# Optimization experiments

Hardware: AMD Instinct MI355X
Metric: run time of the kernel (lower is better)

## Reference

```python
import jax, jax.numpy as jnp
import numpy as np

V, R, D, B, L, M = 10000, 8192, 1024, 1024, 64, 65536


def setup_inputs() -> dict:
    key = jax.random.key(0)
    ks = jax.random.split(key, 10)
    s = 1.0 / np.sqrt(D)
    tokens = jax.random.randint(ks[0], (B, L), 0, V)
    i_idx = jax.random.randint(ks[1], (M,), 0, B * L)
    j_idx = jax.random.randint(ks[2], (M,), 0, B * L)  # stands for j-1 in the original
    r_idx = jax.random.randint(ks[3], (M,), 0, R)
    emb = jax.random.normal(ks[4], (V, D), dtype=jnp.float32) * 0.1
    Wxh = jax.random.normal(ks[5], (D, D), dtype=jnp.float32) * s
    Whh = jax.random.normal(ks[6], (D, D), dtype=jnp.float32) * s
    bh = jnp.zeros((D,), jnp.float32)
    h0 = jnp.zeros((D,), jnp.float32)
    W1 = jax.random.normal(ks[7], (2 * D, D), dtype=jnp.float32) * (1.0 / np.sqrt(2 * D))
    b1 = jnp.zeros((D,), jnp.float32)
    W2 = jax.random.normal(ks[8], (D, R), dtype=jnp.float32) * s
    b2 = jnp.zeros((R,), jnp.float32)
    return dict(tokens=tokens, i_idx=i_idx, j_idx=j_idx, r_idx=r_idx, emb=emb,
                Wxh=Wxh, Whh=Whh, bh=bh, h0=h0, W1=W1, b1=b1, W2=W2, b2=b2)


def reference(tokens, i_idx, j_idx, r_idx, emb, Wxh, Whh, bh, h0, W1, b1, W2, b2):
    # encode: embedding lookup + Elman RNN over time (batched across B sentences)
    x = emb[tokens]                                   # [B, L, D]
    h_init = jnp.broadcast_to(h0, (x.shape[0], h0.shape[0]))

    def step(h, xt):                                  # xt: [B, D]
        h = jnp.tanh(xt @ Wxh + h @ Whh + bh)
        return h, h

    _, hs = jax.lax.scan(step, h_init, jnp.swapaxes(x, 0, 1))  # [L, B, D]
    enc = jnp.swapaxes(hs, 0, 1).reshape(-1, h0.shape[0])      # [B*L, D]

    # batched score_rule over all M tree nodes:
    # cat(enc[i], enc[j-1]) -> tanh(Linear) -> Linear, then index rule r
    c = jnp.concatenate([enc[i_idx], enc[j_idx]], axis=-1)     # [M, 2D]
    h = jnp.tanh(c @ W1 + b1)                                  # [M, D]
    w2_sel = W2.T[r_idx]                                       # [M, D] (only needed logit rows)
    scores = jnp.einsum('md,md->m', h, w2_sel) + b2[r_idx]     # [M]
    return scores
```

## Files before the change

### kernel.cpp

```cpp
#include <hip/hip_runtime.h>

#define D_DIM   1024
#define L_SEQ   64
#define B_BATCH 1024
#define M_NODES 65536
#define R_RULES 8192
#define V_VOCAB 10000

typedef unsigned short bf16_t;
typedef __attribute__((ext_vector_type(8))) short s8v;
typedef __attribute__((ext_vector_type(4))) short s4v;
typedef __attribute__((ext_vector_type(4))) float f4v;

static __device__ __forceinline__ float bf2f(unsigned short u) {
    union { unsigned int i; float f; } v; v.i = ((unsigned int)u) << 16; return v.f;
}
static __device__ __forceinline__ unsigned short f2bf(float f) {
    union { float f; unsigned int i; } v; v.f = f;
    return (unsigned short)((v.i + 0x7FFFu + ((v.i >> 16) & 1u)) >> 16);
}
static __device__ __forceinline__ float fast_tanh(float x) {
    float xc = fminf(fmaxf(x, -15.f), 15.f);
    float t  = __expf(2.f * xc);
    return (t - 1.f) * __builtin_amdgcn_rcpf(t + 1.f);
}

static __device__ __forceinline__ f4v mfma16(s8v a, s8v b, f4v c) {
    return __builtin_amdgcn_mfma_f32_16x16x32_bf16(a, b, c, 0, 0, 0);
}

__global__ __launch_bounds__(256) void k_cvt_emb(
    const float* __restrict__ emb, bf16_t* __restrict__ embB)
{
    size_t i = ((size_t)blockIdx.x * 256 + threadIdx.x) * 8;
    f4v x0 = *(const f4v*)&emb[i];
    f4v x1 = *(const f4v*)&emb[i + 4];
    s8v o;
    o[0] = (short)f2bf(x0.x); o[1] = (short)f2bf(x0.y);
    o[2] = (short)f2bf(x0.z); o[3] = (short)f2bf(x0.w);
    o[4] = (short)f2bf(x1.x); o[5] = (short)f2bf(x1.y);
    o[6] = (short)f2bf(x1.z); o[7] = (short)f2bf(x1.w);
    *(s8v*)&embB[i] = o;
}

__global__ __launch_bounds__(256) void k_transcvt(
    const float* __restrict__ src, bf16_t* __restrict__ dst, int K, int N)
{
    __shared__ float s[32][33];
    int n0 = blockIdx.x * 32, k0 = blockIdx.y * 32;
    int tx = threadIdx.x, ty = threadIdx.y;
#pragma unroll
    for (int i = 0; i < 4; ++i)
        s[ty + i * 8][tx] = src[(size_t)(k0 + ty + i * 8) * N + n0 + tx];
    __syncthreads();
#pragma unroll
    for (int i = 0; i < 4; ++i)
        dst[(size_t)(n0 + ty + i * 8) * K + k0 + tx] = f2bf(s[tx][ty + i * 8]);
}

__global__ __launch_bounds__(256) void k_cvt_h0(
    const float* __restrict__ h0, bf16_t* __restrict__ h0b)
{
    for (int u = threadIdx.x; u < D_DIM; u += 256) h0b[u] = f2bf(h0[u]);
}

__global__ __launch_bounds__(256) void k_xw_mfma(
    const int* __restrict__ tokens, const bf16_t* __restrict__ embB,
    const bf16_t* __restrict__ WxhT, const float* __restrict__ bh,
    bf16_t* __restrict__ XE)
{
    __shared__ bf16_t As[128 * 64];
    __shared__ bf16_t Bs[128 * 64];
    __shared__ float  epi[4][16][68];

    const int bi  = blockIdx.x;
    const int xcd = bi & 7, j = bi >> 3;
    const int row0 = ((xcd << 6) + (j >> 3)) * 128;
    const int col0 = (j & 7) * 128;

    const int tid = threadIdx.x;
    const int w = tid >> 6, l = tid & 63;
    const int q = l >> 4, t16 = l & 15;
    const int wm = (w >> 1) * 64, wn = (w & 1) * 64;

    const int rr = tid >> 2, c0 = tid & 3;
    const int sw0 = ((c0       ^ (rr & 7)) << 3);
    const int sw1 = (((c0 + 4) ^ (rr & 7)) << 3);

    const bf16_t* arow[2];
#pragma unroll
    for (int r = 0; r < 2; ++r)
        arow[r] = embB + (size_t)tokens[row0 + rr + r * 64] * D_DIM + c0 * 8;
    const bf16_t* brow[2];
#pragma unroll
    for (int r = 0; r < 2; ++r)
        brow[r] = WxhT + (size_t)(col0 + rr + r * 64) * D_DIM + c0 * 8;

    f4v acc[4][4];
#pragma unroll
    for (int i = 0; i < 4; ++i)
#pragma unroll
        for (int jj = 0; jj < 4; ++jj) acc[i][jj] = (f4v)0.f;

    s8v a00 = *(const s8v*)(arow[0]);
    s8v a01 = *(const s8v*)(arow[0] + 32);
    s8v a10 = *(const s8v*)(arow[1]);
    s8v a11 = *(const s8v*)(arow[1] + 32);
    s8v b00 = *(const s8v*)(brow[0]);
    s8v b01 = *(const s8v*)(brow[0] + 32);
    s8v b10 = *(const s8v*)(brow[1]);
    s8v b11 = *(const s8v*)(brow[1] + 32);

    const int r7 = t16 & 7;
    for (int k0 = 0; k0 < D_DIM; k0 += 64) {
        __syncthreads();
        *(s8v*)&As[rr * 64 + sw0]        = a00;
        *(s8v*)&As[rr * 64 + sw1]        = a01;
        *(s8v*)&As[(rr + 64) * 64 + sw0] = a10;
        *(s8v*)&As[(rr + 64) * 64 + sw1] = a11;
        *(s8v*)&Bs[rr * 64 + sw0]        = b00;
        *(s8v*)&Bs[rr * 64 + sw1]        = b01;
        *(s8v*)&Bs[(rr + 64) * 64 + sw0] = b10;
        *(s8v*)&Bs[(rr + 64) * 64 + sw1] = b11;
        int kn = k0 + 64;
        if (kn < D_DIM) {
            a00 = *(const s8v*)(arow[0] + kn);
            a01 = *(const s8v*)(arow[0] + kn + 32);
            a10 = *(const s8v*)(arow[1] + kn);
            a11 = *(const s8v*)(arow[1] + kn + 32);
            b00 = *(const s8v*)(brow[0] + kn);
            b01 = *(const s8v*)(brow[0] + kn + 32);
            b10 = *(const s8v*)(brow[1] + kn);
            b11 = *(const s8v*)(brow[1] + kn + 32);
        }
        __syncthreads();
#pragma unroll
        for (int sub = 0; sub < 2; ++sub) {
            const int rsl = (((sub * 4 + q) ^ r7) << 3);
            s8v af[4], bfr[4];
#pragma unroll
            for (int ti = 0; ti < 4; ++ti)
                af[ti] = *(const s8v*)&As[(wm + ti * 16 + t16) * 64 + rsl];
#pragma unroll
            for (int tj = 0; tj < 4; ++tj)
                bfr[tj] = *(const s8v*)&Bs[(wn + tj * 16 + t16) * 64 + rsl];
#pragma unroll
            for (int ti = 0; ti < 4; ++ti)
#pragma unroll
                for (int tj = 0; tj < 4; ++tj)
                    acc[ti][tj] = mfma16(af[ti], bfr[tj], acc[ti][tj]);
        }
    }

    const int lr = l >> 2, c16 = (l & 3) * 16;
    f4v bias[4];
#pragma unroll
    for (int u = 0; u < 4; ++u)
        bias[u] = *(const f4v*)&bh[col0 + wn + c16 + u * 4];
#pragma unroll
    for (int ti = 0; ti < 4; ++ti) {
#pragma unroll
        for (int tj = 0; tj < 4; ++tj)
#pragma unroll
            for (int rg = 0; rg < 4; ++rg)
                epi[w][q * 4 + rg][tj * 16 + t16] = acc[ti][tj][rg];
        s8v o0, o1;
#pragma unroll
        for (int u = 0; u < 8; ++u) {
            o0[u] = (short)f2bf(epi[w][lr][c16 + u]     + bias[u >> 2][u & 3]);
            o1[u] = (short)f2bf(epi[w][lr][c16 + 8 + u] + bias[2 + (u >> 2)][u & 3]);
        }
        size_t orow = (size_t)(row0 + wm + ti * 16 + lr) * D_DIM + col0 + wn + c16;
        *(s8v*)&XE[orow]     = o0;
        *(s8v*)&XE[orow + 8] = o1;
    }
}

__global__ __launch_bounds__(512) void k_step_mfma(
    const bf16_t* __restrict__ Abase, int strideRow,
    const bf16_t* __restrict__ WhhT, bf16_t* __restrict__ XE, int t)
{
    __shared__ bf16_t As[64 * 256];
    __shared__ bf16_t Bs[64 * 256];
    __shared__ float  epi[8][16][36];

    const int tid = threadIdx.x;
    const int w = tid >> 6, l = tid & 63;
    const int q = l >> 4, t16 = l & 15;
    const int wr = w & 3, wc = w >> 2;
    const int row0 = blockIdx.x * 64, col0 = blockIdx.y * 64;

    const int rr = tid >> 3, c0 = tid & 7;
    const int swb = ((c0 ^ (rr & 7)) << 3);

    const bf16_t* asrc = Abase + (size_t)(row0 + rr) * strideRow + c0 * 8;
    const bf16_t* bsrc = WhhT + (size_t)(col0 + rr) * D_DIM + c0 * 8;

    f4v acc[2];
    acc[0] = (f4v)0.f; acc[1] = (f4v)0.f;

    s8v pa[4], pb[4];
#pragma unroll
    for (int kk = 0; kk < 4; ++kk) {
        pa[kk] = *(const s8v*)(asrc + kk * 64);
        pb[kk] = *(const s8v*)(bsrc + kk * 64);
    }

    const int r7 = t16 & 7;
    for (int k0 = 0; k0 < D_DIM; k0 += 256) {
        __syncthreads();
#pragma unroll
        for (int kk = 0; kk < 4; ++kk) {
            *(s8v*)&As[rr * 256 + kk * 64 + swb] = pa[kk];
            *(s8v*)&Bs[rr * 256 + kk * 64 + swb] = pb[kk];
        }
        int kn = k0 + 256;
        if (kn < D_DIM) {
#pragma unroll
            for (int kk = 0; kk < 4; ++kk) {
                pa[kk] = *(const s8v*)(asrc + kn + kk * 64);
                pb[kk] = *(const s8v*)(bsrc + kn + kk * 64);
            }
        }
        __syncthreads();
#pragma unroll
        for (int sub = 0; sub < 8; ++sub) {
            const int slot = sub * 4 + q;
            const int rsl  = ((slot & 24) | ((slot ^ r7) & 7)) << 3;
            s8v af = *(const s8v*)&As[(wr * 16 + t16) * 256 + rsl];
            s8v b0 = *(const s8v*)&Bs[(wc * 32 + t16) * 256 + rsl];
            s8v b1 = *(const s8v*)&Bs[(wc * 32 + 16 + t16) * 256 + rsl];
            acc[0] = mfma16(af, b0, acc[0]);
            acc[1] = mfma16(af, b1, acc[1]);
        }
    }

    const int lr = l >> 2, c8 = (l & 3) * 8;
#pragma unroll
    for (int tj = 0; tj < 2; ++tj)
#pragma unroll
        for (int rg = 0; rg < 4; ++rg)
            epi[w][q * 4 + rg][tj * 16 + t16] = acc[tj][rg];
    f4v v0 = *(const f4v*)&epi[w][lr][c8];
    f4v v1 = *(const f4v*)&epi[w][lr][c8 + 4];
    int b = row0 + wr * 16 + lr;
    size_t xi = ((size_t)b * L_SEQ + t) * D_DIM + col0 + wc * 32 + c8;
    s8v x = *(const s8v*)&XE[xi];
    s8v o;
#pragma unroll
    for (int u = 0; u < 4; ++u) {
        o[u]     = (short)f2bf(fast_tanh(bf2f((unsigned short)x[u])     + v0[u]));
        o[u + 4] = (short)f2bf(fast_tanh(bf2f((unsigned short)x[u + 4]) + v1[u]));
    }
    *(s8v*)&XE[xi] = o;
}

__global__ __launch_bounds__(256) void k_mlp_mfma(
    const int* __restrict__ i_idx, const int* __restrict__ j_idx,
    const bf16_t* __restrict__ XE, const bf16_t* __restrict__ W1T,
    const float* __restrict__ b1, const bf16_t* __restrict__ Wt2,
    const int* __restrict__ r_idx, float* __restrict__ partials)
{
    __shared__ bf16_t As[128 * 64];
    __shared__ bf16_t Bs[128 * 64];

    const int bi  = blockIdx.x;
    const int xcd = bi & 7, j = bi >> 3;
    const int rowTile = (xcd << 6) + (j >> 3);
    const int colTile = j & 7;
    const int row0 = rowTile * 128, col0 = colTile * 128;

    const int tid = threadIdx.x;
    const int w = tid >> 6, l = tid & 63;
    const int q = l >> 4, t16 = l & 15;
    const int wm = (w >> 1) * 64, wn = (w & 1) * 64;

    const int rr = tid >> 2, c0 = tid & 3;
    const int sw0 = ((c0       ^ (rr & 7)) << 3);
    const int sw1 = (((c0 + 4) ^ (rr & 7)) << 3);

    const bf16_t* pi[2]; const bf16_t* pj[2];
#pragma unroll
    for (int r = 0; r < 2; ++r) {
        int m = row0 + rr + r * 64;
        pi[r] = XE + (size_t)i_idx[m] * D_DIM + c0 * 8;
        pj[r] = XE + (size_t)j_idx[m] * D_DIM - D_DIM + c0 * 8;
    }
    const bf16_t* brow[2];
#pragma unroll
    for (int r = 0; r < 2; ++r)
        brow[r] = W1T + (size_t)(col0 + rr + r * 64) * (2 * D_DIM) + c0 * 8;

    f4v acc[4][4];
#pragma unroll
    for (int i = 0; i < 4; ++i)
#pragma unroll
        for (int jj = 0; jj < 4; ++jj) acc[i][jj] = (f4v)0.f;

    s8v a00 = *(const s8v*)(pi[0]);
    s8v a01 = *(const s8v*)(pi[0] + 32);
    s8v a10 = *(const s8v*)(pi[1]);
    s8v a11 = *(const s8v*)(pi[1] + 32);
    s8v b00 = *(const s8v*)(brow[0]);
    s8v b01 = *(const s8v*)(brow[0] + 32);
    s8v b10 = *(const s8v*)(brow[1]);
    s8v b11 = *(const s8v*)(brow[1] + 32);

    const int r7 = t16 & 7;
    for (int k0 = 0; k0 < 2 * D_DIM; k0 += 64) {
        __syncthreads();
        *(s8v*)&As[rr * 64 + sw0]        = a00;
        *(s8v*)&As[rr * 64 + sw1]        = a01;
        *(s8v*)&As[(rr + 64) * 64 + sw0] = a10;
        *(s8v*)&As[(rr + 64) * 64 + sw1] = a11;
        *(s8v*)&Bs[rr * 64 + sw0]        = b00;
        *(s8v*)&Bs[rr * 64 + sw1]        = b01;
        *(s8v*)&Bs[(rr + 64) * 64 + sw0] = b10;
        *(s8v*)&Bs[(rr + 64) * 64 + sw1] = b11;
        int kn = k0 + 64;
        if (kn < 2 * D_DIM) {
            const bf16_t* A0 = (kn < D_DIM) ? pi[0] : pj[0];
            const bf16_t* A1 = (kn < D_DIM) ? pi[1] : pj[1];
            a00 = *(const s8v*)(A0 + kn);
            a01 = *(const s8v*)(A0 + kn + 32);
            a10 = *(const s8v*)(A1 + kn);
            a11 = *(const s8v*)(A1 + kn + 32);
            b00 = *(const s8v*)(brow[0] + kn);
            b01 = *(const s8v*)(brow[0] + kn + 32);
            b10 = *(const s8v*)(brow[1] + kn);
            b11 = *(const s8v*)(brow[1] + kn + 32);
        }
        __syncthreads();
#pragma unroll
        for (int sub = 0; sub < 2; ++sub) {
            const int rsl = (((sub * 4 + q) ^ r7) << 3);
            s8v af[4], bfr[4];
#pragma unroll
            for (int ti = 0; ti < 4; ++ti)
                af[ti] = *(const s8v*)&As[(wm + ti * 16 + t16) * 64 + rsl];
#pragma unroll
            for (int tj = 0; tj < 4; ++tj)
                bfr[tj] = *(const s8v*)&Bs[(wn + tj * 16 + t16) * 64 + rsl];
#pragma unroll
            for (int ti = 0; ti < 4; ++ti)
#pragma unroll
                for (int tj = 0; tj < 4; ++tj)
                    acc[ti][tj] = mfma16(af[ti], bfr[tj], acc[ti][tj]);
        }
    }

    const int cb = colTile * 2 + (w & 1);
#pragma unroll
    for (int ti = 0; ti < 4; ++ti) {
#pragma unroll
        for (int rg = 0; rg < 4; ++rg) {
            int m = row0 + wm + ti * 16 + q * 4 + rg;
            int r = r_idx[m];
            const bf16_t* wrow = Wt2 + (size_t)r * D_DIM + col0 + wn + t16;
            float pd = 0.f;
#pragma unroll
            for (int tj = 0; tj < 4; ++tj) {
                int col = col0 + wn + tj * 16 + t16;
                float h = fast_tanh(acc[ti][tj][rg] + b1[col]);
                pd += h * bf2f(wrow[tj * 16]);
            }
            pd += __shfl_xor(pd, 1);
            pd += __shfl_xor(pd, 2);
            pd += __shfl_xor(pd, 4);
            pd += __shfl_xor(pd, 8);
            if (t16 == 0)
                partials[(size_t)cb * M_NODES + m] = pd;
        }
    }
}

__global__ __launch_bounds__(256) void k_reduce(
    const float* __restrict__ partials, const int* __restrict__ r_idx,
    const float* __restrict__ b2, float* __restrict__ out)
{
    int m = blockIdx.x * 256 + threadIdx.x;
    float s = 0.f;
#pragma unroll
    for (int cb = 0; cb < 16; ++cb)
        s += partials[(size_t)cb * M_NODES + m];
    out[m] = s + b2[r_idx[m]];
}

extern "C" void kernel_launch(void* const* d_in, const int* in_sizes, int n_in,
                              void* d_out, int out_size, void* d_ws, size_t ws_size,
                              hipStream_t stream) {
    const int*   tokens = (const int*)  d_in[0];
    const int*   i_idx  = (const int*)  d_in[1];
    const int*   j_idx  = (const int*)  d_in[2];
    const int*   r_idx  = (const int*)  d_in[3];
    const float* emb    = (const float*)d_in[4];
    const float* Wxh    = (const float*)d_in[5];
    const float* Whh    = (const float*)d_in[6];
    const float* bh     = (const float*)d_in[7];
    const float* h0     = (const float*)d_in[8];
    const float* W1     = (const float*)d_in[9];
    const float* b1     = (const float*)d_in[10];
    const float* W2     = (const float*)d_in[11];
    const float* b2     = (const float*)d_in[12];
    float* out = (float*)d_out;

    bf16_t* XE   = (bf16_t*)d_ws;
    bf16_t* WxhT = XE   + (size_t)M_NODES * D_DIM;
    bf16_t* WhhT = WxhT + (size_t)D_DIM * D_DIM;
    bf16_t* W1T  = WhhT + (size_t)D_DIM * D_DIM;
    bf16_t* Wt2  = W1T  + (size_t)2 * D_DIM * D_DIM;
    bf16_t* embB = WhhT;
    bf16_t* h0b  = Wt2  + (size_t)R_RULES * D_DIM;
    float*  par  = (float*)(h0b + 2048);

    k_cvt_emb<<<V_VOCAB * D_DIM / 2048, 256, 0, stream>>>(emb, embB);
    k_transcvt<<<dim3(D_DIM / 32, D_DIM / 32), dim3(32, 8), 0, stream>>>(Wxh, WxhT, D_DIM, D_DIM);
    k_cvt_h0<<<1, 256, 0, stream>>>(h0, h0b);

    k_xw_mfma<<<4096, 256, 0, stream>>>(tokens, embB, WxhT, bh, XE);

    k_transcvt<<<dim3(D_DIM / 32, D_DIM / 32), dim3(32, 8), 0, stream>>>(Whh, WhhT, D_DIM, D_DIM);
    k_transcvt<<<dim3(D_DIM / 32, 2 * D_DIM / 32), dim3(32, 8), 0, stream>>>(W1, W1T, 2 * D_DIM, D_DIM);
    k_transcvt<<<dim3(R_RULES / 32, D_DIM / 32), dim3(32, 8), 0, stream>>>(W2, Wt2, D_DIM, R_RULES);

    for (int t = 0; t < L_SEQ; ++t) {
        const bf16_t* Abase = (t == 0) ? h0b : (XE + (size_t)(t - 1) * D_DIM);
        int strideRow       = (t == 0) ? 0   : L_SEQ * D_DIM;
        k_step_mfma<<<dim3(B_BATCH / 64, D_DIM / 64), 512, 0, stream>>>(
            Abase, strideRow, WhhT, XE, t);
    }

    k_mlp_mfma<<<4096, 256, 0, stream>>>(
        i_idx, j_idx, XE, W1T, b1, Wt2, r_idx, par);

    k_reduce<<<M_NODES / 256, 256, 0, stream>>>(par, r_idx, b2, out);
}
```

Before: 1.198 ms.

## Fuse RNN timesteps into one persistent cooperative kernel with register-resident Whh

Replaces 64 per-timestep kernel launches with a single cooperative persistent kernel of 256 blocks. Each block keeps its 128-column slice of Whh in registers for the whole sequence and synchronises with the other blocks sharing its row group through a global atomic counter. This removes per-step launch overhead and the repeated reloading of Whh from memory. In exchange it adds spin-wait barrier latency, heavy register pressure, and depends on all blocks being co-resident.

Result: slower. 1.293 ms (+7.9%).

```diff
diff --git a/kernel.cpp b/kernel.cpp
--- a/kernel.cpp
+++ b/kernel.cpp
@@ -6,6 +6,7 @@
 #define M_NODES 65536
 #define R_RULES 8192
 #define V_VOCAB 10000
+#define NBLK_RNN 256
 
 typedef unsigned short bf16_t;
 typedef __attribute__((ext_vector_type(8))) short s8v;
@@ -59,8 +60,9 @@
 }
 
 __global__ __launch_bounds__(256) void k_cvt_h0(
-    const float* __restrict__ h0, bf16_t* __restrict__ h0b)
-{
+    const float* __restrict__ h0, bf16_t* __restrict__ h0b, int* __restrict__ bars)
+{
+    if (threadIdx.x < 32) bars[threadIdx.x * 16] = 0;
     for (int u = threadIdx.x; u < D_DIM; u += 256) h0b[u] = f2bf(h0[u]);
 }
 
@@ -176,83 +178,92 @@
     }
 }
 
-__global__ __launch_bounds__(512) void k_step_mfma(
-    const bf16_t* __restrict__ Abase, int strideRow,
-    const bf16_t* __restrict__ WhhT, bf16_t* __restrict__ XE, int t)
-{
-    __shared__ bf16_t As[64 * 256];
-    __shared__ bf16_t Bs[64 * 256];
-    __shared__ float  epi[8][16][36];
+__global__ __launch_bounds__(512, 2) void k_rnn(
+    const bf16_t* __restrict__ h0b, const bf16_t* __restrict__ WhhT,
+    bf16_t* __restrict__ XE, int* __restrict__ bars)
+{
+    __shared__ bf16_t As[32 * 128];
+    __shared__ float  epi[8][16][20];
+
+    const int bx  = blockIdx.x;
+    const int rgp = bx & 31;
+    const int cgp = bx >> 5;
+    const int row0 = rgp * 32;
+    const int col0 = cgp * 128;
 
     const int tid = threadIdx.x;
     const int w = tid >> 6, l = tid & 63;
     const int q = l >> 4, t16 = l & 15;
-    const int wr = w & 3, wc = w >> 2;
-    const int row0 = blockIdx.x * 64, col0 = blockIdx.y * 64;
-
-    const int rr = tid >> 3, c0 = tid & 7;
-    const int swb = ((c0 ^ (rr & 7)) << 3);
-
-    const bf16_t* asrc = Abase + (size_t)(row0 + rr) * strideRow + c0 * 8;
-    const bf16_t* bsrc = WhhT + (size_t)(col0 + rr) * D_DIM + c0 * 8;
-
-    f4v acc[2];
-    acc[0] = (f4v)0.f; acc[1] = (f4v)0.f;
-
-    s8v pa[4], pb[4];
-#pragma unroll
-    for (int kk = 0; kk < 4; ++kk) {
-        pa[kk] = *(const s8v*)(asrc + kk * 64);
-        pb[kk] = *(const s8v*)(bsrc + kk * 64);
-    }
-
-    const int r7 = t16 & 7;
-    for (int k0 = 0; k0 < D_DIM; k0 += 256) {
-        __syncthreads();
-#pragma unroll
-        for (int kk = 0; kk < 4; ++kk) {
-            *(s8v*)&As[rr * 256 + kk * 64 + swb] = pa[kk];
-            *(s8v*)&Bs[rr * 256 + kk * 64 + swb] = pb[kk];
-        }
-        int kn = k0 + 256;
-        if (kn < D_DIM) {
+
+    s8v breg[32];
+    {
+        const bf16_t* bp = WhhT + (size_t)(col0 + w * 16 + t16) * D_DIM + q * 8;
+#pragma unroll
+        for (int ks = 0; ks < 32; ++ks)
+            breg[ks] = *(const s8v*)(bp + ks * 32);
+#pragma unroll
+        for (int ks = 0; ks < 32; ++ks)
+            asm volatile("" : "+v"(breg[ks]));
+    }
+
+    const int ar = tid >> 4, aslot = tid & 15;
+    bf16_t* awr = As + ar * 128 + ((aslot ^ (ar & 7)) << 3);
+    const int rx = t16 & 7;
+    const bf16_t* ard0 = As + t16 * 128;
+    const bf16_t* ard1 = As + (16 + t16) * 128;
+
+    const size_t xrowA = (size_t)(row0 + ar) * (L_SEQ * D_DIM) + aslot * 8;
+    const int lr = l >> 2, c4 = (l & 3) * 4;
+
+    int* bar = bars + rgp * 16;
+
+    for (int t = 0; t < L_SEQ; ++t) {
+        const bf16_t* asrc = (t == 0) ? (h0b + aslot * 8)
+                                      : (XE + xrowA + (size_t)(t - 1) * D_DIM);
+        f4v acc0 = (f4v)0.f, acc1 = (f4v)0.f;
+        s8v rA = *(const s8v*)asrc;
+#pragma unroll
+        for (int cch = 0; cch < 8; ++cch) {
+            __syncthreads();
+            *(s8v*)awr = rA;
+            if (cch < 7) rA = *(const s8v*)(asrc + (cch + 1) * 128);
+            __syncthreads();
 #pragma unroll
             for (int kk = 0; kk < 4; ++kk) {
-                pa[kk] = *(const s8v*)(asrc + kn + kk * 64);
-                pb[kk] = *(const s8v*)(bsrc + kn + kk * 64);
+                const int sl = ((kk * 4 + q) ^ rx) << 3;
+                s8v a0 = *(const s8v*)(ard0 + sl);
+                s8v a1 = *(const s8v*)(ard1 + sl);
+                acc0 = mfma16(a0, breg[cch * 4 + kk], acc0);
+                acc1 = mfma16(a1, breg[cch * 4 + kk], acc1);
             }
         }
-        __syncthreads();
-#pragma unroll
-        for (int sub = 0; sub < 8; ++sub) {
-            const int slot = sub * 4 + q;
-            const int rsl  = ((slot & 24) | ((slot ^ r7) & 7)) << 3;
-            s8v af = *(const s8v*)&As[(wr * 16 + t16) * 256 + rsl];
-            s8v b0 = *(const s8v*)&Bs[(wc * 32 + t16) * 256 + rsl];
-            s8v b1 = *(const s8v*)&Bs[(wc * 32 + 16 + t16) * 256 + rsl];
-            acc[0] = mfma16(af, b0, acc[0]);
-            acc[1] = mfma16(af, b1, acc[1]);
-        }
-    }
-
-    const int lr = l >> 2, c8 = (l & 3) * 8;
-#pragma unroll
-    for (int tj = 0; tj < 2; ++tj)
-#pragma unroll
-        for (int rg = 0; rg < 4; ++rg)
-            epi[w][q * 4 + rg][tj * 16 + t16] = acc[tj][rg];
-    f4v v0 = *(const f4v*)&epi[w][lr][c8];
-    f4v v1 = *(const f4v*)&epi[w][lr][c8 + 4];
-    int b = row0 + wr * 16 + lr;
-    size_t xi = ((size_t)b * L_SEQ + t) * D_DIM + col0 + wc * 32 + c8;
-    s8v x = *(const s8v*)&XE[xi];
-    s8v o;
-#pragma unroll
-    for (int u = 0; u < 4; ++u) {
-        o[u]     = (short)f2bf(fast_tanh(bf2f((unsigned short)x[u])     + v0[u]));
-        o[u + 4] = (short)f2bf(fast_tanh(bf2f((unsigned short)x[u + 4]) + v1[u]));
-    }
-    *(s8v*)&XE[xi] = o;
+#pragma unroll
+        for (int ti = 0; ti < 2; ++ti) {
+            f4v a = (ti == 0) ? acc0 : acc1;
+#pragma unroll
+            for (int rgi = 0; rgi < 4; ++rgi)
+                epi[w][q * 4 + rgi][t16] = a[rgi];
+            f4v v = *(const f4v*)&epi[w][lr][c4];
+            int b = row0 + ti * 16 + lr;
+            size_t xi = ((size_t)b * L_SEQ + t) * D_DIM + col0 + w * 16 + c4;
+            s4v x = *(const s4v*)&XE[xi];
+            s4v o;
+#pragma unroll
+            for (int u = 0; u < 4; ++u)
+                o[u] = (short)f2bf(fast_tanh(bf2f((unsigned short)x[u]) + v[u]));
+            *(s4v*)&XE[xi] = o;
+        }
+        if (t < L_SEQ - 1) {
+            __syncthreads();
+            if (tid == 0) {
+                __hip_atomic_fetch_add(bar, 1, __ATOMIC_RELEASE, __HIP_MEMORY_SCOPE_AGENT);
+                const int target = 8 * (t + 1);
+                while (__hip_atomic_load(bar, __ATOMIC_RELAXED, __HIP_MEMORY_SCOPE_AGENT) < target)
+                    __builtin_amdgcn_s_sleep(1);
+            }
+            __syncthreads();
+        }
+    }
 }
 
 __global__ __launch_bounds__(256) void k_mlp_mfma(
@@ -411,11 +422,12 @@
     bf16_t* Wt2  = W1T  + (size_t)2 * D_DIM * D_DIM;
     bf16_t* embB = WhhT;
     bf16_t* h0b  = Wt2  + (size_t)R_RULES * D_DIM;
+    int*    bars = (int*)(h0b + 1024);
     float*  par  = (float*)(h0b + 2048);
 
     k_cvt_emb<<<V_VOCAB * D_DIM / 2048, 256, 0, stream>>>(emb, embB);
     k_transcvt<<<dim3(D_DIM / 32, D_DIM / 32), dim3(32, 8), 0, stream>>>(Wxh, WxhT, D_DIM, D_DIM);
-    k_cvt_h0<<<1, 256, 0, stream>>>(h0, h0b);
+    k_cvt_h0<<<1, 256, 0, stream>>>(h0, h0b, bars);
 
     k_xw_mfma<<<4096, 256, 0, stream>>>(tokens, embB, WxhT, bh, XE);
 
@@ -423,11 +435,10 @@
     k_transcvt<<<dim3(D_DIM / 32, 2 * D_DIM / 32), dim3(32, 8), 0, stream>>>(W1, W1T, 2 * D_DIM, D_DIM);
     k_transcvt<<<dim3(R_RULES / 32, D_DIM / 32), dim3(32, 8), 0, stream>>>(W2, Wt2, D_DIM, R_RULES);
 
-    for (int t = 0; t < L_SEQ; ++t) {
-        const bf16_t* Abase = (t == 0) ? h0b : (XE + (size_t)(t - 1) * D_DIM);
-        int strideRow       = (t == 0) ? 0   : L_SEQ * D_DIM;
-        k_step_mfma<<<dim3(B_BATCH / 64, D_DIM / 64), 512, 0, stream>>>(
-            Abase, strideRow, WhhT, XE, t);
+    {
+        void* args[] = { (void*)&h0b, (void*)&WhhT, (void*)&XE, (void*)&bars };
+        hipLaunchCooperativeKernel((const void*)k_rnn, dim3(NBLK_RNN), dim3(512),
+                                   args, 0, stream);
     }
 
     k_mlp_mfma<<<4096, 256, 0, stream>>>(
```
